# Performance work log

Measured on AMD Instinct MI355X. Metric: run time of the kernel, lower is better.

The kernel has to match this reference:

```python
import jax, jax.numpy as jnp
import numpy as np

D_MODEL = 1024
NHEAD = 16
EPS = 1e-5


def pos_embed(x, pos):
    # Faithful, vectorized form of the sparse rotation matrix in the source.
    # Source builds rot[..., i, i+1] = sin(pos*i*omega) for even i and
    # rot[..., i, i-1] = cos(pos*i*omega) for odd i, then contracts the feature
    # dim of x against the rotation (intended einsum 'btf,btfd->btd').
    # Resulting column j: even j <- x[..., j+1]*cos(pos*(j+1)*omega),
    #                     odd  j <- x[..., j-1]*sin(pos*(j-1)*omega).
    d = x.shape[-1]
    omega = jnp.pi / d
    i_even = jnp.arange(0, d, 2, dtype=x.dtype)   # even rows -> odd output cols (sin)
    i_odd = jnp.arange(1, d, 2, dtype=x.dtype)    # odd rows  -> even output cols (cos)
    p = pos[..., None]  # (L,B,1)
    sin_part = jnp.sin(p * i_even * omega) * x[..., 0::2]  # -> odd columns
    cos_part = jnp.cos(p * i_odd * omega) * x[..., 1::2]   # -> even columns
    # interleave: even col = cos_part, odd col = sin_part
    return jnp.stack([cos_part, sin_part], axis=-1).reshape(x.shape)


def layer_norm_eps(x, w, b):
    # Source uses torch.var default (unbiased, ddof=1)
    mean = jnp.mean(x, axis=-1, keepdims=True)
    var = jnp.var(x, axis=-1, keepdims=True, ddof=1)
    return w * (x - mean) / jnp.sqrt(var + EPS) + b


def mha(q, k, v, w_qkv, b_qkv, w_o, b_o, nhead):
    L, B, E = q.shape
    S = k.shape[0]
    hd = E // nhead
    wq, wk, wv = jnp.split(w_qkv, 3, axis=0)
    bq, bk, bv = jnp.split(b_qkv, 3, axis=0)
    qp = (q @ wq.T + bq).reshape(L, B, nhead, hd).transpose(1, 2, 0, 3)  # (B,h,L,hd)
    kp = (k @ wk.T + bk).reshape(S, B, nhead, hd).transpose(1, 2, 0, 3)
    vp = (v @ wv.T + bv).reshape(S, B, nhead, hd).transpose(1, 2, 0, 3)
    scale = jnp.asarray(1.0 / np.sqrt(hd), q.dtype)
    scores = jnp.einsum('bhld,bhsd->bhls', qp, kp) * scale
    attn = jax.nn.softmax(scores, axis=-1)
    out = jnp.einsum('bhls,bhsd->bhld', attn, vp)
    out = out.transpose(2, 0, 1, 3).reshape(L, B, E) @ w_o.T + b_o
    ws = attn.mean(axis=1)  # average over heads, torch default
    return out, ws


def setup_inputs() -> dict:
    key = jax.random.key(0)
    ks = jax.random.split(key, 16)
    T, S, B, E, FF = 1024, 1024, 4, D_MODEL, 4096
    sd = 0.02
    return {
        'tgt': jax.random.normal(ks[0], (T, B, E), jnp.float32),
        'memory': jax.random.normal(ks[1], (S, B, E), jnp.float32),
        'pos': jax.random.uniform(ks[2], (S, B), jnp.float32) * S,
        'query_pos': jax.random.uniform(ks[3], (T, B), jnp.float32) * T,
        'w_qkv_self': jax.random.normal(ks[4], (3 * E, E), jnp.float32) * sd,
        'b_qkv_self': jnp.zeros((3 * E,), jnp.float32),
        'w_o_self': jax.random.normal(ks[5], (E, E), jnp.float32) * sd,
        'b_o_self': jnp.zeros((E,), jnp.float32),
        'w_qkv_cross': jax.random.normal(ks[6], (3 * E, E), jnp.float32) * sd,
        'b_qkv_cross': jnp.zeros((3 * E,), jnp.float32),
        'w_o_cross': jax.random.normal(ks[7], (E, E), jnp.float32) * sd,
        'b_o_cross': jnp.zeros((E,), jnp.float32),
        'w1': jax.random.normal(ks[8], (FF, E), jnp.float32) * sd,
        'b1': jnp.zeros((FF,), jnp.float32),
        'w2': jax.random.normal(ks[9], (E, FF), jnp.float32) * sd,
        'b2': jnp.zeros((E,), jnp.float32),
        'g1': jnp.ones((E,), jnp.float32),
        'beta1': jnp.zeros((E,), jnp.float32),
        'g2': jnp.ones((E,), jnp.float32),
        'beta2': jnp.zeros((E,), jnp.float32),
    }


def reference(tgt, memory, pos, query_pos,
              w_qkv_self, b_qkv_self, w_o_self, b_o_self,
              w_qkv_cross, b_qkv_cross, w_o_cross, b_o_cross,
              w1, b1, w2, b2, g1, beta1, g2, beta2):
    # normalize_before=False, residual=True, dropout inactive (eval)
    qk = pos_embed(tgt, query_pos)
    tgt2, _ = mha(qk, qk, tgt, w_qkv_self, b_qkv_self, w_o_self, b_o_self, NHEAD)
    tgt = tgt + tgt2
    tgt = layer_norm_eps(tgt, g1, beta1)
    tgt2, ws = mha(pos_embed(tgt, query_pos), pos_embed(memory, pos), memory,
                   w_qkv_cross, b_qkv_cross, w_o_cross, b_o_cross, NHEAD)
    tgt = tgt + tgt2
    tgt = layer_norm_eps(tgt, g2, beta2)
    tgt2 = jax.nn.relu(tgt @ w1.T + b1) @ w2.T + b2
    tgt = tgt + tgt2
    return tgt, ws
```

## Files before the change

### kernel.cpp

```cpp
#include <hip/hip_runtime.h>

typedef unsigned short u16;
typedef __attribute__((ext_vector_type(8))) short short8;
typedef __attribute__((ext_vector_type(8))) unsigned short u16x8;
typedef __attribute__((ext_vector_type(4))) float f32x4;

#define GLOAD16(SRC, DST) __builtin_amdgcn_global_load_lds( \
    (const __attribute__((address_space(1))) void*)(SRC),   \
    (__attribute__((address_space(3))) void*)(DST), 16, 0, 0)

#define SWZ(BKv, r) ((BKv) == 32 ? (((r) >> 1) & 3) : ((r) & 7))

__device__ __forceinline__ u16 f2bf(float f) {
  union { float f; unsigned u; } v; v.f = f;
  unsigned r = v.u + 0x7fffu + ((v.u >> 16) & 1u);
  return (u16)(r >> 16);
}
__device__ __forceinline__ float bf2f(u16 h) {
  union { unsigned u; float f; } v; v.u = ((unsigned)h) << 16;
  return v.f;
}

__global__ __launch_bounds__(256) void wcvt_kernel(const float* __restrict__ s0,
                                                   const float* __restrict__ s1,
                                                   const float* __restrict__ s2,
                                                   const float* __restrict__ s3,
                                                   const float* __restrict__ s4,
                                                   const float* __restrict__ s5,
                                                   u16* __restrict__ dst) {
  long i = ((long)blockIdx.x * 256 + threadIdx.x) * 4;
  const float* src; long off;
  if (i < 3145728)        { src = s0; off = 0; }
  else if (i < 4194304)   { src = s1; off = 3145728; }
  else if (i < 7340032)   { src = s2; off = 4194304; }
  else if (i < 8388608)   { src = s3; off = 7340032; }
  else if (i < 12582912)  { src = s4; off = 8388608; }
  else                    { src = s5; off = 12582912; }
  float4 v = *(const float4*)(src + (i - off));
  ushort4 o; o.x = f2bf(v.x); o.y = f2bf(v.y); o.z = f2bf(v.z); o.w = f2bf(v.w);
  *(ushort4*)(dst + i) = o;
}

__global__ __launch_bounds__(256) void pos_embed_kernel(const float* __restrict__ x,
                                                        const float* __restrict__ pos,
                                                        u16* __restrict__ out,
                                                        u16* __restrict__ out2,
                                                        u16* __restrict__ raw) {
  int m = blockIdx.x;
  int tid = threadIdx.x;
  float p = pos[m];
  long base = ((long)m << 10);
  int j = tid * 4;
  float4 xv = *(const float4*)(x + base + j);
  const float inv = 1.0f / 2048.0f;
  float r0 = p * (float)(j + 0) * inv;
  float r1 = p * (float)(j + 1) * inv;
  float r2 = p * (float)(j + 2) * inv;
  float r3 = p * (float)(j + 3) * inv;
  float s1 = __builtin_amdgcn_sinf(r0 - floorf(r0));
  float c0 = __builtin_amdgcn_cosf(r1 - floorf(r1));
  float s3 = __builtin_amdgcn_sinf(r2 - floorf(r2));
  float c2 = __builtin_amdgcn_cosf(r3 - floorf(r3));
  ushort4 o;
  o.x = f2bf(c0 * xv.y);
  o.y = f2bf(s1 * xv.x);
  o.z = f2bf(c2 * xv.w);
  o.w = f2bf(s3 * xv.z);
  *(ushort4*)(out + base + j) = o;
  if (out2) *(ushort4*)(out2 + base + j) = o;
  if (raw) {
    ushort4 rw; rw.x = f2bf(xv.x); rw.y = f2bf(xv.y); rw.z = f2bf(xv.z); rw.w = f2bf(xv.w);
    *(ushort4*)(raw + base + j) = rw;
  }
}

__global__ __launch_bounds__(256) void split_qkv_kernel(const u16* __restrict__ P,
                                                        u16* __restrict__ Qb,
                                                        u16* __restrict__ Kb,
                                                        u16* __restrict__ Vtb) {
  long e = ((long)blockIdx.x * 256 + threadIdx.x) * 8;
  int m = (int)(e / 3072);
  int n = (int)(e % 3072);
  int t = m >> 2, b = m & 3;
  int sec = n >> 10, nn = n & 1023;
  int h = nn >> 6, d = nn & 63;
  long bh = b * 16 + h;
  u16x8 v = *(const u16x8*)(P + e);
  if (sec == 0) {
    *(u16x8*)(Qb + (bh << 16) + ((long)t << 6) + d) = v;
  } else if (sec == 1) {
    *(u16x8*)(Kb + (bh << 16) + ((long)t << 6) + d) = v;
  } else {
    u16* dst = Vtb + (bh << 16) + ((long)d << 10) + t;
#pragma unroll
    for (int q = 0; q < 8; q++) dst[(long)q << 10] = v[q];
  }
}

__global__ __launch_bounds__(256) void fattn_kernel(const u16* __restrict__ Q,
                                                    const u16* __restrict__ K,
                                                    const u16* __restrict__ Vt,
                                                    u16* __restrict__ AO,
                                                    float2* __restrict__ Ml) {
  __shared__ u16 lK[2][4096];
  __shared__ u16 lV[2][4096];
  __shared__ u16 lP[4096];
  const int tid = threadIdx.x, lane = tid & 63, wid = tid >> 6;
  const int nb = gridDim.x * gridDim.y;
  const int orig = blockIdx.y * gridDim.x + blockIdx.x;
  const int swz = (orig & 7) * (nb >> 3) + (orig >> 3);
  const int qt = swz & 15;
  const int bh = swz >> 4;
  const int b = bh >> 4, h = bh & 15;
  const u16* Qp = Q + ((long)bh << 16);
  const u16* Kp = K + ((long)bh << 16);
  const u16* Vp = Vt + ((long)bh << 16);
  const int q0 = qt << 6;
  const int cr = lane >> 4;

  short8 af0, af1;
  {
    const u16* qs = Qp + (long)(q0 + wid * 16 + (lane & 15)) * 64 + cr * 8;
    af0 = *(const short8*)qs;
    af1 = *(const short8*)(qs + 32);
  }

  float m[4] = {-1e30f, -1e30f, -1e30f, -1e30f};
  float l[4] = {0.f, 0.f, 0.f, 0.f};
  f32x4 acco[4] = {};

  auto stage = [&](int bufi, int kv) {
    int s0 = kv << 6;
#pragma unroll
    for (int it = 0; it < 2; it++) {
      int c = it * 256 + tid;
      int row = c >> 3, ch = c & 7;
      int sch = (ch ^ (row & 7)) * 8;
      GLOAD16(Kp + (long)(s0 + row) * 64 + sch, &lK[bufi][c * 8]);
      GLOAD16(Vp + (long)row * 1024 + s0 + sch, &lV[bufi][c * 8]);
    }
  };

  stage(0, 0);
  __syncthreads();
  int buf = 0;
  for (int kv = 0; kv < 16; kv++) {
    if (kv < 15) stage(buf ^ 1, kv + 1);
    f32x4 accs[4];
#pragma unroll
    for (int j = 0; j < 4; j++) {
      int sr = j * 16 + (lane & 15);
      const short8 kf0 = *(const short8*)&lK[buf][sr * 64 + ((cr ^ (sr & 7)) * 8)];
      const short8 kf1 = *(const short8*)&lK[buf][sr * 64 + (((4 + cr) ^ (sr & 7)) * 8)];
      f32x4 zz = {};
      zz = __builtin_amdgcn_mfma_f32_16x16x32_bf16(af0, kf0, zz, 0, 0, 0);
      accs[j] = __builtin_amdgcn_mfma_f32_16x16x32_bf16(af1, kf1, zz, 0, 0, 0);
    }
    float tm[4], rs[4];
#pragma unroll
    for (int r = 0; r < 4; r++) {
      float a0 = accs[0][r] * 0.125f, a1 = accs[1][r] * 0.125f;
      float a2 = accs[2][r] * 0.125f, a3 = accs[3][r] * 0.125f;
      accs[0][r] = a0; accs[1][r] = a1; accs[2][r] = a2; accs[3][r] = a3;
      tm[r] = fmaxf(fmaxf(a0, a1), fmaxf(a2, a3));
    }
#pragma unroll
    for (int o = 1; o < 16; o <<= 1)
#pragma unroll
      for (int r = 0; r < 4; r++) tm[r] = fmaxf(tm[r], __shfl_xor(tm[r], o));
#pragma unroll
    for (int r = 0; r < 4; r++) {
      float mn = fmaxf(m[r], tm[r]);
      float f = __expf(m[r] - mn);
      m[r] = mn;
      l[r] *= f;
      acco[0][r] *= f; acco[1][r] *= f; acco[2][r] *= f; acco[3][r] *= f;
      rs[r] = 0.f;
    }
#pragma unroll
    for (int j = 0; j < 4; j++)
#pragma unroll
      for (int r = 0; r < 4; r++) {
        float p = __expf(accs[j][r] - m[r]);
        accs[j][r] = p;
        rs[r] += p;
      }
#pragma unroll
    for (int o = 1; o < 16; o <<= 1)
#pragma unroll
      for (int r = 0; r < 4; r++) rs[r] += __shfl_xor(rs[r], o);
#pragma unroll
    for (int r = 0; r < 4; r++) l[r] += rs[r];
    u16* pw = &lP[wid * 1024];
#pragma unroll
    for (int j = 0; j < 4; j++)
#pragma unroll
      for (int r = 0; r < 4; r++) {
        int qr = (lane >> 4) * 4 + r;
        int s = j * 16 + (lane & 15);
        pw[qr * 64 + (((s >> 3) ^ (qr & 7)) * 8) + (s & 7)] = f2bf(accs[j][r]);
      }
    {
      int ql = lane & 15;
      const u16* pr = &lP[wid * 1024 + ql * 64];
      short8 pa0 = *(const short8*)&pr[(cr ^ (ql & 7)) * 8];
      short8 pa1 = *(const short8*)&pr[((4 + cr) ^ (ql & 7)) * 8];
#pragma unroll
      for (int j = 0; j < 4; j++) {
        int dr = j * 16 + (lane & 15);
        const short8 vf0 = *(const short8*)&lV[buf][dr * 64 + ((cr ^ (dr & 7)) * 8)];
        const short8 vf1 = *(const short8*)&lV[buf][dr * 64 + (((4 + cr) ^ (dr & 7)) * 8)];
        acco[j] = __builtin_amdgcn_mfma_f32_16x16x32_bf16(pa0, vf0, acco[j], 0, 0, 0);
        acco[j] = __builtin_amdgcn_mfma_f32_16x16x32_bf16(pa1, vf1, acco[j], 0, 0, 0);
      }
    }
    __syncthreads();
    buf ^= 1;
  }
  float invl[4];
#pragma unroll
  for (int r = 0; r < 4; r++) invl[r] = 1.0f / l[r];
#pragma unroll
  for (int j = 0; j < 4; j++)
#pragma unroll
    for (int r = 0; r < 4; r++) {
      int t = q0 + wid * 16 + (lane >> 4) * 4 + r;
      int e = (b << 10) + (h << 6) + j * 16 + (lane & 15);
      AO[(long)t * 4096 + e] = f2bf(acco[j][r] * invl[r]);
    }
  if (Ml && (lane & 15) == 0) {
#pragma unroll
    for (int r = 0; r < 4; r++) {
      int t = q0 + wid * 16 + (lane >> 4) * 4 + r;
      Ml[((long)bh << 10) + t] = make_float2(m[r], invl[r]);
    }
  }
}

__global__ __launch_bounds__(256) void wsrec_kernel(const u16* __restrict__ Q,
                                                    const u16* __restrict__ K,
                                                    const float2* __restrict__ Ml,
                                                    float* __restrict__ ws) {
  __shared__ u16 lK[2][4096];
  const int tid = threadIdx.x, lane = tid & 63, wid = tid >> 6;
  const int nb = gridDim.x * gridDim.y;
  const int orig = blockIdx.y * gridDim.x + blockIdx.x;
  const int swz = (orig & 7) * (nb >> 3) + (orig >> 3);
  const int st = swz & 15, lt = swz >> 4;
  const int b = blockIdx.z;
  const int s0 = st << 6, l0 = lt << 6;
  const int cr = lane >> 4;

  auto stage = [&](int bufi, int h) {
    const u16* Kp = K + (((long)(b * 16 + h)) << 16);
#pragma unroll
    for (int it = 0; it < 2; it++) {
      int c = it * 256 + tid;
      int row = c >> 3, ch = c & 7;
      GLOAD16(Kp + (long)(s0 + row) * 64 + ((ch ^ (row & 7)) * 8), &lK[bufi][c * 8]);
    }
  };

  f32x4 wacc[4] = {};
  stage(0, 0);
  __syncthreads();
  int buf = 0;
  for (int h = 0; h < 16; h++) {
    if (h < 15) stage(buf ^ 1, h + 1);
    const int bh = b * 16 + h;
    short8 af0, af1;
    {
      const u16* qs = Q + ((long)bh << 16) + (long)(l0 + wid * 16 + (lane & 15)) * 64 + cr * 8;
      af0 = *(const short8*)qs;
      af1 = *(const short8*)(qs + 32);
    }
    f32x4 accs[4];
#pragma unroll
    for (int j = 0; j < 4; j++) {
      int sr = j * 16 + (lane & 15);
      const short8 kf0 = *(const short8*)&lK[buf][sr * 64 + ((cr ^ (sr & 7)) * 8)];
      const short8 kf1 = *(const short8*)&lK[buf][sr * 64 + (((4 + cr) ^ (sr & 7)) * 8)];
      f32x4 zz = {};
      zz = __builtin_amdgcn_mfma_f32_16x16x32_bf16(af0, kf0, zz, 0, 0, 0);
      accs[j] = __builtin_amdgcn_mfma_f32_16x16x32_bf16(af1, kf1, zz, 0, 0, 0);
    }
    float mm[4], il[4];
#pragma unroll
    for (int r = 0; r < 4; r++) {
      float2 v = Ml[((long)bh << 10) + l0 + wid * 16 + (lane >> 4) * 4 + r];
      mm[r] = v.x; il[r] = v.y * 0.0625f;
    }
#pragma unroll
    for (int j = 0; j < 4; j++)
#pragma unroll
      for (int r = 0; r < 4; r++)
        wacc[j][r] += __expf(accs[j][r] * 0.125f - mm[r]) * il[r];
    __syncthreads();
    buf ^= 1;
  }
#pragma unroll
  for (int j = 0; j < 4; j++)
#pragma unroll
    for (int r = 0; r < 4; r++) {
      int li = l0 + wid * 16 + (lane >> 4) * 4 + r;
      int si = s0 + j * 16 + (lane & 15);
      ws[((long)b << 20) + (long)li * 1024 + si] = wacc[j][r];
    }
}

__global__ __launch_bounds__(256) void ln_kernel(const float* __restrict__ X,
                                                 const float* __restrict__ D1,
                                                 const float* __restrict__ D2,
                                                 const float* __restrict__ bo,
                                                 const float* __restrict__ g,
                                                 const float* __restrict__ be,
                                                 float* __restrict__ out,
                                                 u16* __restrict__ bfout) {
  int mrow = blockIdx.x;
  int tid = threadIdx.x, lane = tid & 63, wid = tid >> 6;
  long base = ((long)mrow << 10);
  float4 a = *(const float4*)(X + base + tid * 4);
  float4 b = *(const float4*)(D1 + base + tid * 4);
  float x0 = a.x + b.x, x1 = a.y + b.y, x2 = a.z + b.z, x3 = a.w + b.w;
  if (D2) {
    float4 c = *(const float4*)(D2 + base + tid * 4);
    x0 += c.x; x1 += c.y; x2 += c.z; x3 += c.w;
  }
  if (bo) {
    float4 c = *(const float4*)(bo + tid * 4);
    x0 += c.x; x1 += c.y; x2 += c.z; x3 += c.w;
  }
  float s = x0 + x1 + x2 + x3;
#pragma unroll
  for (int o = 32; o; o >>= 1) s += __shfl_xor(s, o);
  __shared__ float red[4];
  if (lane == 0) red[wid] = s;
  __syncthreads();
  float mean = (red[0] + red[1] + red[2] + red[3]) * (1.0f / 1024.0f);
  float d0 = x0 - mean, d1 = x1 - mean, d2 = x2 - mean, d3 = x3 - mean;
  float ss = d0 * d0 + d1 * d1 + d2 * d2 + d3 * d3;
#pragma unroll
  for (int o = 32; o; o >>= 1) ss += __shfl_xor(ss, o);
  __syncthreads();
  if (lane == 0) red[wid] = ss;
  __syncthreads();
  float var = (red[0] + red[1] + red[2] + red[3]) * (1.0f / 1023.0f);
  float sc = 1.0f / sqrtf(var + 1e-5f);
  float4 gv = *(const float4*)(g + tid * 4);
  float4 bv = *(const float4*)(be + tid * 4);
  float y0 = gv.x * d0 * sc + bv.x;
  float y1 = gv.y * d1 * sc + bv.y;
  float y2 = gv.z * d2 * sc + bv.z;
  float y3 = gv.w * d3 * sc + bv.w;
  float4 o4; o4.x = y0; o4.y = y1; o4.z = y2; o4.w = y3;
  *(float4*)(out + base + tid * 4) = o4;
  if (bfout) {
    ushort4 hh; hh.x = f2bf(y0); hh.y = f2bf(y1); hh.z = f2bf(y2); hh.w = f2bf(y3);
    *(ushort4*)(bfout + base + tid * 4) = hh;
  }
}

__global__ __launch_bounds__(256) void add3_kernel(const float* __restrict__ X,
                                                   const float* __restrict__ P0,
                                                   const float* __restrict__ P1,
                                                   const float* __restrict__ b,
                                                   float* __restrict__ out) {
  long i = ((long)blockIdx.x * 256 + threadIdx.x) * 4;
  int col = (int)(i & 1023);
  float4 x = *(const float4*)(X + i);
  float4 p = *(const float4*)(P0 + i);
  float4 q = *(const float4*)(P1 + i);
  float4 bb = *(const float4*)(b + col);
  float4 o;
  o.x = x.x + p.x + q.x + bb.x;
  o.y = x.y + p.y + q.y + bb.y;
  o.z = x.z + p.z + q.z + bb.z;
  o.w = x.w + p.w + q.w + bb.w;
  *(float4*)(out + i) = o;
}

template <int BM, int BN, int BK, int WR, int WC, int NT, int DB>
__global__ __launch_bounds__(NT)
void gemm_bt_kernel(const u16* __restrict__ A, const u16* __restrict__ B,
                    void* __restrict__ C, const float* __restrict__ bias,
                    int lda, int ldb, int ldc, int K,
                    long sAz, long sBz, long sCz, long sbz,
                    float alpha, int flags) {
  constexpr int WTM = BM / WR, WTN = BN / WC;
  constexpr int FM = WTM / 16, FN = WTN / 16;
  constexpr int NC = BK / 8;
  __shared__ u16 lA[DB][BM * BK];
  __shared__ u16 lB[DB][BN * BK];
  const int tid = threadIdx.x, lane = tid & 63, wid = tid >> 6;
  const int wr = wid / WC, wc = wid % WC;
  const int z = blockIdx.z;

  const int nwg = gridDim.x * gridDim.y;
  const int orig = blockIdx.y * gridDim.x + blockIdx.x;
  const int qq = nwg >> 3, rr = nwg & 7;
  const int xcd = orig & 7, idx = orig >> 3;
  const int swz = (xcd < rr ? xcd * (qq + 1) : rr * (qq + 1) + (xcd - rr) * qq) + idx;
  const int bxs = swz % gridDim.x;
  const int bys = swz / gridDim.x;

  const u16* Ab = A + z * sAz + (long)bys * BM * lda;
  const u16* Bb = B + z * sBz + (long)bxs * BN * ldb;

  f32x4 acc[FM][FN] = {};

  auto stage = [&](int bufi, int k0) {
#pragma unroll
    for (int c0 = 0; c0 < BM * NC; c0 += NT) {
      int c = c0 + tid;
      if ((BM * NC) % NT == 0 || c < BM * NC) {
        int row = c / NC, ch = c % NC;
        int sch = ch ^ SWZ(BK, row);
        GLOAD16(Ab + (long)row * lda + k0 + sch * 8, &lA[bufi][c * 8]);
      }
    }
#pragma unroll
    for (int c0 = 0; c0 < BN * NC; c0 += NT) {
      int c = c0 + tid;
      if ((BN * NC) % NT == 0 || c < BN * NC) {
        int row = c / NC, ch = c % NC;
        int sch = ch ^ SWZ(BK, row);
        GLOAD16(Bb + (long)row * ldb + k0 + sch * 8, &lB[bufi][c * 8]);
      }
    }
  };

  auto compute = [&](int bufi) {
#pragma unroll
    for (int kk = 0; kk < BK / 32; kk++) {
      short8 afv[FM], bfv[FN];
#pragma unroll
      for (int i = 0; i < FM; i++) {
        int row = wr * WTM + i * 16 + (lane & 15);
        int ch = kk * 4 + (lane >> 4);
        afv[i] = *(const short8*)&lA[bufi][row * BK + ((ch ^ SWZ(BK, row)) * 8)];
      }
#pragma unroll
      for (int j = 0; j < FN; j++) {
        int row = wc * WTN + j * 16 + (lane & 15);
        int ch = kk * 4 + (lane >> 4);
        bfv[j] = *(const short8*)&lB[bufi][row * BK + ((ch ^ SWZ(BK, row)) * 8)];
      }
#pragma unroll
      for (int i = 0; i < FM; i++)
#pragma unroll
        for (int j = 0; j < FN; j++)
          acc[i][j] = __builtin_amdgcn_mfma_f32_16x16x32_bf16(afv[i], bfv[j], acc[i][j], 0, 0, 0);
    }
  };

  const int nk = K / BK;
  if (DB == 2) {
    stage(0, 0);
    __syncthreads();
    int cur = 0;
    for (int t = 0; t < nk; t++) {
      if (t + 1 < nk) stage(cur ^ 1, (t + 1) * BK);
      compute(cur);
      __syncthreads();
      cur ^= 1;
    }
  } else {
    for (int t = 0; t < nk; t++) {
      stage(0, t * BK);
      __syncthreads();
      compute(0);
      __syncthreads();
    }
  }

  const long rbase = (long)bys * BM + wr * WTM;
  const int cbase = bxs * BN + wc * WTN;
  const float* bz = bias ? (bias + z * sbz) : nullptr;
#pragma unroll
  for (int i = 0; i < FM; i++)
#pragma unroll
    for (int j = 0; j < FN; j++)
#pragma unroll
      for (int r = 0; r < 4; r++) {
        long row = rbase + i * 16 + ((lane >> 4) * 4 + r);
        int col = cbase + j * 16 + (lane & 15);
        float v = acc[i][j][r] * alpha;
        if (flags & 1) v += bz[col];
        if (flags & 2) v = fmaxf(v, 0.0f);
        long off = (long)z * sCz + row * (long)ldc + col;
        if (flags & 4) ((float*)C)[off] = v;
        else ((u16*)C)[off] = f2bf(v);
      }
}

extern "C" void kernel_launch(void* const* d_in, const int* in_sizes, int n_in,
                              void* d_out, int out_size, void* d_ws, size_t ws_size,
                              hipStream_t stream) {
  const float* tgt  = (const float*)d_in[0];
  const float* mem  = (const float*)d_in[1];
  const float* pos  = (const float*)d_in[2];
  const float* qpos = (const float*)d_in[3];
  const float* wqkvS = (const float*)d_in[4];
  const float* bqkvS = (const float*)d_in[5];
  const float* woS   = (const float*)d_in[6];
  const float* boS   = (const float*)d_in[7];
  const float* wqkvC = (const float*)d_in[8];
  const float* bqkvC = (const float*)d_in[9];
  const float* woC   = (const float*)d_in[10];
  const float* boC   = (const float*)d_in[11];
  const float* w1  = (const float*)d_in[12];
  const float* b1  = (const float*)d_in[13];
  const float* w2  = (const float*)d_in[14];
  const float* b2  = (const float*)d_in[15];
  const float* g1  = (const float*)d_in[16];
  const float* be1 = (const float*)d_in[17];
  const float* g2  = (const float*)d_in[18];
  const float* be2 = (const float*)d_in[19];

  const size_t MB = 1024ull * 1024ull;
  float* out0 = (float*)d_out;
  float* wsout = out0 + 4194304;

  char* W = (char*)d_ws;
  u16* wb = (u16*)W;
  u16* wqkvS_b = wb;
  u16* woS_b   = wb + 3145728;
  u16* wqkvC_b = wb + 4194304;
  u16* woC_b   = wb + 7340032;
  u16* w1_b    = wb + 8388608;
  u16* w2_b    = wb + 12582912;
  float* Xf   = (float*)(W + 32 * MB);
  float* OPar = (float*)(W + 48 * MB);
  u16* Pq  = (u16*)(W + 48 * MB);
  u16* bf1 = (u16*)(W + 80 * MB);
  u16* bf2 = (u16*)(W + 88 * MB);
  u16* bf3 = (u16*)(W + 96 * MB);
  float2* Ml = (float2*)(W + 96 * MB);
  u16* Qb  = (u16*)(W + 104 * MB);
  u16* Kb  = (u16*)(W + 112 * MB);
  u16* Vtb = (u16*)(W + 120 * MB);
  u16* AOb = (u16*)(W + 128 * MB);
  u16* F1  = (u16*)(W + 104 * MB);

  wcvt_kernel<<<16384, 256, 0, stream>>>(wqkvS, woS, wqkvC, woC, w1, w2, wb);

  pos_embed_kernel<<<4096, 256, 0, stream>>>(tgt, qpos, bf1, bf2, bf3);
  gemm_bt_kernel<128, 128, 32, 2, 4, 512, 2><<<dim3(8, 32, 3), 512, 0, stream>>>(
      bf1, wqkvS_b, Pq, bqkvS, 1024, 1024, 3072, 1024,
      4194304, 1048576, 1024, 1024, 1.0f, 1);
  split_qkv_kernel<<<6144, 256, 0, stream>>>(Pq, Qb, Kb, Vtb);
  fattn_kernel<<<dim3(16, 64), 256, 0, stream>>>(Qb, Kb, Vtb, AOb, nullptr);
  gemm_bt_kernel<128, 128, 32, 2, 4, 512, 2><<<dim3(8, 32, 2), 512, 0, stream>>>(
      AOb, woS_b, OPar, nullptr, 1024, 1024, 1024, 512,
      512, 512, 4194304, 0, 1.0f, 4);
  ln_kernel<<<4096, 256, 0, stream>>>(tgt, OPar, OPar + 4194304, boS, g1, be1, Xf, nullptr);

  pos_embed_kernel<<<4096, 256, 0, stream>>>(Xf, qpos, bf1, nullptr, nullptr);
  pos_embed_kernel<<<4096, 256, 0, stream>>>(mem, pos, bf2, nullptr, bf3);
  gemm_bt_kernel<128, 128, 32, 2, 4, 512, 2><<<dim3(8, 32, 3), 512, 0, stream>>>(
      bf1, wqkvC_b, Pq, bqkvC, 1024, 1024, 3072, 1024,
      4194304, 1048576, 1024, 1024, 1.0f, 1);
  split_qkv_kernel<<<6144, 256, 0, stream>>>(Pq, Qb, Kb, Vtb);
  fattn_kernel<<<dim3(16, 64), 256, 0, stream>>>(Qb, Kb, Vtb, AOb, Ml);
  wsrec_kernel<<<dim3(16, 16, 4), 256, 0, stream>>>(Qb, Kb, Ml, wsout);
  gemm_bt_kernel<128, 128, 32, 2, 4, 512, 2><<<dim3(8, 32, 2), 512, 0, stream>>>(
      AOb, woC_b, OPar, nullptr, 1024, 1024, 1024, 512,
      512, 512, 4194304, 0, 1.0f, 4);
  ln_kernel<<<4096, 256, 0, stream>>>(Xf, OPar, OPar + 4194304, boC, g2, be2, Xf, bf1);

  gemm_bt_kernel<128, 128, 32, 2, 4, 512, 2><<<dim3(32, 32, 1), 512, 0, stream>>>(
      bf1, w1_b, F1, b1, 1024, 1024, 4096, 1024, 0, 0, 0, 0, 1.0f, 1 | 2);
  gemm_bt_kernel<128, 128, 32, 2, 4, 512, 2><<<dim3(8, 32, 2), 512, 0, stream>>>(
      F1, w2_b, OPar, nullptr, 4096, 4096, 1024, 2048,
      2048, 2048, 4194304, 0, 1.0f, 4);
  add3_kernel<<<4096, 256, 0, stream>>>(Xf, OPar, OPar + 4194304, b2, out0);
}
```

Baseline: 477.4 us.

## Fold softmax scale into Q projection, use exp2, lazy rescale, read K/V directly

The attention and ws-reconstruction kernels stop staging K and V through LDS with double buffering. Each wave now loads K and V fragments straight from global memory, which removes the block-wide barriers. The scale 0.125*log2(e) is folded into the Q projection GEMM epilogue (applied after bias, only for the z==0 Q slice), so the kernels can use hardware exp2 with no per-score multiply. The running-max rescale is skipped unless some row's max grows by more than 8, and P is packed to bf16 with v_cvt_pk_bf16_f32. The trade is more redundant global/L2 traffic for K/V across the four waves, plus reduced numerical headroom from the lazy rescale.

```diff
diff --git a/kernel.cpp b/kernel.cpp
--- a/kernel.cpp
+++ b/kernel.cpp
@@ -10,6 +10,8 @@
     (__attribute__((address_space(3))) void*)(DST), 16, 0, 0)
 
 #define SWZ(BKv, r) ((BKv) == 32 ? (((r) >> 1) & 3) : ((r) & 7))
+
+#define QSCALE 0.18033688011112042f
 
 __device__ __forceinline__ u16 f2bf(float f) {
   union { float f; unsigned u; } v; v.f = f;
@@ -102,9 +104,7 @@
                                                     const u16* __restrict__ Vt,
                                                     u16* __restrict__ AO,
                                                     float2* __restrict__ Ml) {
-  __shared__ u16 lK[2][4096];
-  __shared__ u16 lV[2][4096];
-  __shared__ u16 lP[4096];
+  __shared__ u16 lP[4][1024];
   const int tid = threadIdx.x, lane = tid & 63, wid = tid >> 6;
   const int nb = gridDim.x * gridDim.y;
   const int orig = blockIdx.y * gridDim.x + blockIdx.x;
@@ -129,59 +129,44 @@
   float l[4] = {0.f, 0.f, 0.f, 0.f};
   f32x4 acco[4] = {};
 
-  auto stage = [&](int bufi, int kv) {
-    int s0 = kv << 6;
-#pragma unroll
-    for (int it = 0; it < 2; it++) {
-      int c = it * 256 + tid;
-      int row = c >> 3, ch = c & 7;
-      int sch = (ch ^ (row & 7)) * 8;
-      GLOAD16(Kp + (long)(s0 + row) * 64 + sch, &lK[bufi][c * 8]);
-      GLOAD16(Vp + (long)row * 1024 + s0 + sch, &lV[bufi][c * 8]);
-    }
-  };
-
-  stage(0, 0);
-  __syncthreads();
-  int buf = 0;
   for (int kv = 0; kv < 16; kv++) {
-    if (kv < 15) stage(buf ^ 1, kv + 1);
+    const int s0 = kv << 6;
     f32x4 accs[4];
 #pragma unroll
     for (int j = 0; j < 4; j++) {
-      int sr = j * 16 + (lane & 15);
-      const short8 kf0 = *(const short8*)&lK[buf][sr * 64 + ((cr ^ (sr & 7)) * 8)];
-      const short8 kf1 = *(const short8*)&lK[buf][sr * 64 + (((4 + cr) ^ (sr & 7)) * 8)];
+      int sr = s0 + j * 16 + (lane & 15);
+      const u16* ks = Kp + (long)sr * 64 + cr * 8;
+      short8 kf0 = *(const short8*)ks;
+      short8 kf1 = *(const short8*)(ks + 32);
       f32x4 zz = {};
       zz = __builtin_amdgcn_mfma_f32_16x16x32_bf16(af0, kf0, zz, 0, 0, 0);
       accs[j] = __builtin_amdgcn_mfma_f32_16x16x32_bf16(af1, kf1, zz, 0, 0, 0);
     }
-    float tm[4], rs[4];
-#pragma unroll
-    for (int r = 0; r < 4; r++) {
-      float a0 = accs[0][r] * 0.125f, a1 = accs[1][r] * 0.125f;
-      float a2 = accs[2][r] * 0.125f, a3 = accs[3][r] * 0.125f;
-      accs[0][r] = a0; accs[1][r] = a1; accs[2][r] = a2; accs[3][r] = a3;
-      tm[r] = fmaxf(fmaxf(a0, a1), fmaxf(a2, a3));
-    }
+    float tm[4];
+#pragma unroll
+    for (int r = 0; r < 4; r++)
+      tm[r] = fmaxf(fmaxf(accs[0][r], accs[1][r]), fmaxf(accs[2][r], accs[3][r]));
 #pragma unroll
     for (int o = 1; o < 16; o <<= 1)
 #pragma unroll
       for (int r = 0; r < 4; r++) tm[r] = fmaxf(tm[r], __shfl_xor(tm[r], o));
-#pragma unroll
-    for (int r = 0; r < 4; r++) {
-      float mn = fmaxf(m[r], tm[r]);
-      float f = __expf(m[r] - mn);
-      m[r] = mn;
-      l[r] *= f;
-      acco[0][r] *= f; acco[1][r] *= f; acco[2][r] *= f; acco[3][r] *= f;
-      rs[r] = 0.f;
-    }
+    float growth = fmaxf(fmaxf(tm[0] - m[0], tm[1] - m[1]),
+                         fmaxf(tm[2] - m[2], tm[3] - m[3]));
+    if (!__all(growth <= 8.0f)) {
+#pragma unroll
+      for (int r = 0; r < 4; r++) {
+        float mn = fmaxf(m[r], tm[r]);
+        float f = __builtin_amdgcn_exp2f(m[r] - mn);
+        m[r] = mn; l[r] *= f;
+        acco[0][r] *= f; acco[1][r] *= f; acco[2][r] *= f; acco[3][r] *= f;
+      }
+    }
+    float rs[4] = {0.f, 0.f, 0.f, 0.f};
 #pragma unroll
     for (int j = 0; j < 4; j++)
 #pragma unroll
       for (int r = 0; r < 4; r++) {
-        float p = __expf(accs[j][r] - m[r]);
+        float p = __builtin_amdgcn_exp2f(accs[j][r] - m[r]);
         accs[j][r] = p;
         rs[r] += p;
       }
@@ -191,31 +176,36 @@
       for (int r = 0; r < 4; r++) rs[r] += __shfl_xor(rs[r], o);
 #pragma unroll
     for (int r = 0; r < 4; r++) l[r] += rs[r];
-    u16* pw = &lP[wid * 1024];
-#pragma unroll
-    for (int j = 0; j < 4; j++)
+    u16* pw = lP[wid];
+#pragma unroll
+    for (int jp = 0; jp < 2; jp++)
 #pragma unroll
       for (int r = 0; r < 4; r++) {
         int qr = (lane >> 4) * 4 + r;
-        int s = j * 16 + (lane & 15);
-        pw[qr * 64 + (((s >> 3) ^ (qr & 7)) * 8) + (s & 7)] = f2bf(accs[j][r]);
-      }
+        unsigned pk;
+        asm("v_cvt_pk_bf16_f32 %0, %1, %2"
+            : "=v"(pk) : "v"(accs[2 * jp][r]), "v"(accs[2 * jp + 1][r]));
+        int sA = (2 * jp) * 16 + (lane & 15);
+        int sB = sA + 16;
+        pw[qr * 64 + (((sA >> 3) ^ (qr & 7)) * 8) + (sA & 7)] = (u16)pk;
+        pw[qr * 64 + (((sB >> 3) ^ (qr & 7)) * 8) + (sB & 7)] = (u16)(pk >> 16);
+      }
+    asm volatile("s_waitcnt lgkmcnt(0)" ::: "memory");
     {
       int ql = lane & 15;
-      const u16* pr = &lP[wid * 1024 + ql * 64];
+      const u16* pr = &lP[wid][ql * 64];
       short8 pa0 = *(const short8*)&pr[(cr ^ (ql & 7)) * 8];
       short8 pa1 = *(const short8*)&pr[((4 + cr) ^ (ql & 7)) * 8];
 #pragma unroll
       for (int j = 0; j < 4; j++) {
         int dr = j * 16 + (lane & 15);
-        const short8 vf0 = *(const short8*)&lV[buf][dr * 64 + ((cr ^ (dr & 7)) * 8)];
-        const short8 vf1 = *(const short8*)&lV[buf][dr * 64 + (((4 + cr) ^ (dr & 7)) * 8)];
+        const u16* vs = Vp + (long)dr * 1024 + s0 + cr * 8;
+        short8 vf0 = *(const short8*)vs;
+        short8 vf1 = *(const short8*)(vs + 32);
         acco[j] = __builtin_amdgcn_mfma_f32_16x16x32_bf16(pa0, vf0, acco[j], 0, 0, 0);
         acco[j] = __builtin_amdgcn_mfma_f32_16x16x32_bf16(pa1, vf1, acco[j], 0, 0, 0);
       }
     }
-    __syncthreads();
-    buf ^= 1;
   }
   float invl[4];
 #pragma unroll
@@ -241,7 +231,6 @@
                                                     const u16* __restrict__ K,
                                                     const float2* __restrict__ Ml,
                                                     float* __restrict__ ws) {
-  __shared__ u16 lK[2][4096];
   const int tid = threadIdx.x, lane = tid & 63, wid = tid >> 6;
   const int nb = gridDim.x * gridDim.y;
   const int orig = blockIdx.y * gridDim.x + blockIdx.x;
@@ -251,35 +240,20 @@
   const int s0 = st << 6, l0 = lt << 6;
   const int cr = lane >> 4;
 
-  auto stage = [&](int bufi, int h) {
-    const u16* Kp = K + (((long)(b * 16 + h)) << 16);
-#pragma unroll
-    for (int it = 0; it < 2; it++) {
-      int c = it * 256 + tid;
-      int row = c >> 3, ch = c & 7;
-      GLOAD16(Kp + (long)(s0 + row) * 64 + ((ch ^ (row & 7)) * 8), &lK[bufi][c * 8]);
-    }
-  };
-
   f32x4 wacc[4] = {};
-  stage(0, 0);
-  __syncthreads();
-  int buf = 0;
   for (int h = 0; h < 16; h++) {
-    if (h < 15) stage(buf ^ 1, h + 1);
     const int bh = b * 16 + h;
-    short8 af0, af1;
-    {
-      const u16* qs = Q + ((long)bh << 16) + (long)(l0 + wid * 16 + (lane & 15)) * 64 + cr * 8;
-      af0 = *(const short8*)qs;
-      af1 = *(const short8*)(qs + 32);
-    }
+    const u16* qs = Q + ((long)bh << 16) + (long)(l0 + wid * 16 + (lane & 15)) * 64 + cr * 8;
+    short8 af0 = *(const short8*)qs;
+    short8 af1 = *(const short8*)(qs + 32);
+    const u16* Kp = K + ((long)bh << 16);
     f32x4 accs[4];
 #pragma unroll
     for (int j = 0; j < 4; j++) {
-      int sr = j * 16 + (lane & 15);
-      const short8 kf0 = *(const short8*)&lK[buf][sr * 64 + ((cr ^ (sr & 7)) * 8)];
-      const short8 kf1 = *(const short8*)&lK[buf][sr * 64 + (((4 + cr) ^ (sr & 7)) * 8)];
+      int sr = s0 + j * 16 + (lane & 15);
+      const u16* ks = Kp + (long)sr * 64 + cr * 8;
+      short8 kf0 = *(const short8*)ks;
+      short8 kf1 = *(const short8*)(ks + 32);
       f32x4 zz = {};
       zz = __builtin_amdgcn_mfma_f32_16x16x32_bf16(af0, kf0, zz, 0, 0, 0);
       accs[j] = __builtin_amdgcn_mfma_f32_16x16x32_bf16(af1, kf1, zz, 0, 0, 0);
@@ -294,9 +268,7 @@
     for (int j = 0; j < 4; j++)
 #pragma unroll
       for (int r = 0; r < 4; r++)
-        wacc[j][r] += __expf(accs[j][r] * 0.125f - mm[r]) * il[r];
-    __syncthreads();
-    buf ^= 1;
+        wacc[j][r] += __builtin_amdgcn_exp2f(accs[j][r] - mm[r]) * il[r];
   }
 #pragma unroll
   for (int j = 0; j < 4; j++)
@@ -484,8 +456,10 @@
       for (int r = 0; r < 4; r++) {
         long row = rbase + i * 16 + ((lane >> 4) * 4 + r);
         int col = cbase + j * 16 + (lane & 15);
-        float v = acc[i][j][r] * alpha;
+        float v = acc[i][j][r];
+        if (!(flags & 8)) v *= alpha;
         if (flags & 1) v += bz[col];
+        if ((flags & 8) && z == 0) v *= alpha;
         if (flags & 2) v = fmaxf(v, 0.0f);
         long off = (long)z * sCz + row * (long)ldc + col;
         if (flags & 4) ((float*)C)[off] = v;
@@ -547,7 +521,7 @@
   pos_embed_kernel<<<4096, 256, 0, stream>>>(tgt, qpos, bf1, bf2, bf3);
   gemm_bt_kernel<128, 128, 32, 2, 4, 512, 2><<<dim3(8, 32, 3), 512, 0, stream>>>(
       bf1, wqkvS_b, Pq, bqkvS, 1024, 1024, 3072, 1024,
-      4194304, 1048576, 1024, 1024, 1.0f, 1);
+      4194304, 1048576, 1024, 1024, QSCALE, 1 | 8);
   split_qkv_kernel<<<6144, 256, 0, stream>>>(Pq, Qb, Kb, Vtb);
   fattn_kernel<<<dim3(16, 64), 256, 0, stream>>>(Qb, Kb, Vtb, AOb, nullptr);
   gemm_bt_kernel<128, 128, 32, 2, 4, 512, 2><<<dim3(8, 32, 2), 512, 0, stream>>>(
@@ -559,7 +533,7 @@
   pos_embed_kernel<<<4096, 256, 0, stream>>>(mem, pos, bf2, nullptr, bf3);
   gemm_bt_kernel<128, 128, 32, 2, 4, 512, 2><<<dim3(8, 32, 3), 512, 0, stream>>>(
       bf1, wqkvC_b, Pq, bqkvC, 1024, 1024, 3072, 1024,
-      4194304, 1048576, 1024, 1024, 1.0f, 1);
+      4194304, 1048576, 1024, 1024, QSCALE, 1 | 8);
   split_qkv_kernel<<<6144, 256, 0, stream>>>(Pq, Qb, Kb, Vtb);
   fattn_kernel<<<dim3(16, 64), 256, 0, stream>>>(Qb, Kb, Vtb, AOb, Ml);
   wsrec_kernel<<<dim3(16, 16, 4), 256, 0, stream>>>(Qb, Kb, Ml, wsout);
```

New measurement: 647.3 us. +35.6%, slower.
